# Optimization experiments

Hardware: AMD Instinct MI355X
Metric: run time of the kernel (lower is better)

The kernel has to match this reference:

```python
import jax, jax.numpy as jnp
import numpy as np

B, GRID, IN_CO, OUT_CO = 32, 4096, 64, 64
T_EMB, N_MODES = 256, 512
M_HALF = N_MODES // 2 + 1  # 257 retained rFFT modes


def setup_inputs() -> dict:
    key = jax.random.key(0)
    ks = jax.random.split(key, 6)
    w_std = jnp.sqrt(1.0 / (2.0 * IN_CO))
    return {
        "x": jax.random.normal(ks[0], (B, GRID, IN_CO), jnp.float32),
        "t_emb": jax.random.normal(ks[1], (B, T_EMB), jnp.float32),
        "weights_real": jax.random.normal(ks[2], (M_HALF, IN_CO, OUT_CO), jnp.float32) * w_std,
        "weights_imag": jax.random.normal(ks[3], (M_HALF, IN_CO, OUT_CO), jnp.float32) * w_std,
        "dense_real": jax.random.normal(ks[4], (T_EMB, M_HALF), jnp.float32) * jnp.sqrt(1.0 / T_EMB),
        "dense_imag": jax.random.normal(ks[5], (T_EMB, M_HALF), jnp.float32) * jnp.sqrt(1.0 / T_EMB),
    }


def reference(x, t_emb, weights_real, weights_imag, dense_real, dense_imag):
    b, in_grid_sz, _ = x.shape
    m = weights_real.shape[0]  # n_modes//2 + 1
    weights = weights_real + 1j * weights_imag  # (m, in_co, out_co)
    # rFFT over the grid axis
    x_ft = jnp.fft.rfft(x, axis=-2, norm="forward")  # (b, grid//2+1, in_co) complex
    # time modulation per mode: Dense(real) + i*Dense(imag)
    t_tr = (t_emb @ dense_real) + 1j * (t_emb @ dense_imag)  # (b, m)
    # original einsum with eye == elementwise per-mode scale then per-mode matmul
    x_out = jnp.einsum("bmi,mio->bmo", x_ft[:, :m, :], weights) * t_tr[:, :, None]
    out_ft = jnp.zeros((b, in_grid_sz // 2 + 1, weights.shape[-1]), jnp.complex64)
    out_ft = out_ft.at[:, :m, :].set(x_out)
    return jnp.fft.irfft(out_ft, axis=-2, n=in_grid_sz, norm="forward")
```

## Files before the change

### kernel.cpp

```cpp
#include <hip/hip_runtime.h>
#include <hip/hip_bf16.h>

typedef short short8 __attribute__((ext_vector_type(8)));
typedef float f32x4 __attribute__((ext_vector_type(4)));
typedef const void __attribute__((address_space(1))) as1_void;
typedef void __attribute__((address_space(3))) as3_void;

__device__ __forceinline__ float sin_rev(float r) {
  float o; asm("v_sin_f32 %0, %1" : "=v"(o) : "v"(r)); return o;
}
__device__ __forceinline__ float cos_rev(float r) {
  float o; asm("v_cos_f32 %0, %1" : "=v"(o) : "v"(r)); return o;
}

#define INV4096 0.000244140625f
#define INV16   0.0625f

__global__ __launch_bounds__(256) void prep_kernel(__hip_bfloat16* __restrict__ F2,
                                                   __hip_bfloat16* __restrict__ Gm,
                                                   const float* __restrict__ t_emb,
                                                   const float* __restrict__ dr,
                                                   const float* __restrict__ di,
                                                   float* __restrict__ Sr,
                                                   float* __restrict__ Si,
                                                   const float* __restrict__ x,
                                                   __hip_bfloat16* __restrict__ X2T,
                                                   float* __restrict__ Xr256p) {
  const int bid = blockIdx.x;
  const int tid = threadIdx.x;
  __shared__ float te[256];
  __shared__ float tile[64][65];
  __shared__ float red[4][64];

  if (bid < 512) {
    const int row = bid;
    const int m   = (row < 256) ? row : (row - 255);
    const bool is_cos = (row < 256);
#pragma unroll
    for (int it = 0; it < 2; ++it) {
      int n0 = it * 2048 + tid * 8;
      union { short8 v; unsigned short u[8]; } pk;
#pragma unroll
      for (int j = 0; j < 8; ++j) {
        int ph = (m * (n0 + j)) & 4095;
        float v = is_cos ?  cos_rev((float)ph * INV4096)
                         : -sin_rev((float)ph * INV4096);
        __hip_bfloat16 h = __float2bfloat16(v);
        pk.u[j] = *(unsigned short*)&h;
      }
      *(short8*)&F2[(size_t)row * 4096 + n0] = pk.v;
    }
  } else if (bid < 1024) {
    const int nb = (bid - 512) * 8;
#pragma unroll
    for (int it = 0; it < 2; ++it) {
      int e  = it * 2048 + tid * 8;
      int n  = nb + (e >> 9);
      int k0 = e & 511;
      union { short8 v; unsigned short u[8]; } pk;
#pragma unroll
      for (int j = 0; j < 8; ++j) {
        int kk = k0 + j;
        int m  = (kk < 256) ? kk : (kk - 255);
        int ph = (m * n) & 4095;
        float v = (kk < 256) ?  cos_rev((float)ph * INV4096)
                             : -sin_rev((float)ph * INV4096);
        __hip_bfloat16 h = __float2bfloat16(v);
        pk.u[j] = *(unsigned short*)&h;
      }
      *(short8*)&Gm[(size_t)n * 512 + k0] = pk.v;
    }
  } else if (bid < 1056) {
    int b = bid - 1024;
    te[tid] = t_emb[b * 256 + tid];
    __syncthreads();
    for (int m = tid; m < 257; m += 256) {
      float ar = 0.f, ai = 0.f;
      for (int t = 0; t < 256; ++t) {
        float e = te[t];
        ar += e * dr[t * 257 + m];
        ai += e * di[t * 257 + m];
      }
      float c = (m == 0 ? 1.0f : 2.0f) * (1.0f / 4096.0f);
      Sr[b * 257 + m] = ar * c;
      Si[b * 257 + m] = ai * c;
    }
  } else {
    int idx = bid - 1056;
    int nt = idx & 63;
    int b  = idx >> 6;
    int n0 = nt * 64;
#pragma unroll
    for (int it = 0; it < 4; ++it) {
      int c = it * 256 + tid;
      int r = c >> 4, i4 = (c & 15) * 4;
      float4 v = *(const float4*)&x[((size_t)b * 4096 + n0 + r) * 64 + i4];
      tile[r][i4 + 0] = v.x; tile[r][i4 + 1] = v.y;
      tile[r][i4 + 2] = v.z; tile[r][i4 + 3] = v.w;
    }
    __syncthreads();
#pragma unroll
    for (int it = 0; it < 2; ++it) {
      int c  = it * 256 + tid;
      int i  = c >> 3;
      int ch = c & 7;
      union { short8 v; unsigned short u[8]; } pk;
#pragma unroll
      for (int j = 0; j < 8; ++j) {
        __hip_bfloat16 h = __float2bfloat16(tile[ch * 8 + j][i]);
        pk.u[j] = *(unsigned short*)&h;
      }
      *(short8*)&X2T[((size_t)b * 64 + i) * 4096 + n0 + ch * 8] = pk.v;
    }
    {
      int i = tid & 63, g = tid >> 6;
      float acc = 0.f;
#pragma unroll
      for (int j = 0; j < 16; ++j)
        acc += cos_rev((float)j * INV16) * tile[g * 16 + j][i];
      red[g][i] = acc;
    }
    __syncthreads();
    if (tid < 64) {
      Xr256p[((size_t)b * 64 + nt) * 64 + tid] =
          red[0][tid] + red[1][tid] + red[2][tid] + red[3][tid];
    }
  }
}

__device__ __forceinline__ void gemm_core(const __hip_bfloat16* __restrict__ A, int lda, int m0,
                                          const __hip_bfloat16* __restrict__ B, int ldb, int n0,
                                          int k0, int ksteps,
                                          __hip_bfloat16* As, __hip_bfloat16* Bs,
                                          f32x4 acc[4][4]) {
  const int tid  = threadIdx.x;
  const int lane = tid & 63;
  const int wv   = tid >> 6;
  const int wr   = (wv >> 1) * 64;
  const int wc   = (wv & 1) * 64;
  const int fr   = lane & 15;
  const int fq   = lane >> 4;

  for (int ks = 0; ks < ksteps; ++ks) {
    int kt = k0 + ks * 64;
#pragma unroll
    for (int j = 0; j < 4; ++j) {
      int c   = j * 256 + tid;
      int row = c >> 3;
      int chg = (c & 7) ^ (row & 7);
      const __hip_bfloat16* ga = A + (size_t)(m0 + row) * lda + kt + chg * 8;
      const __hip_bfloat16* gb = B + (size_t)(n0 + row) * ldb + kt + chg * 8;
      __hip_bfloat16* la = As + (size_t)(j * 256 + (tid & 192)) * 8;
      __hip_bfloat16* lb = Bs + (size_t)(j * 256 + (tid & 192)) * 8;
      __builtin_amdgcn_global_load_lds((as1_void*)ga, (as3_void*)la, 16, 0, 0);
      __builtin_amdgcn_global_load_lds((as1_void*)gb, (as3_void*)lb, 16, 0, 0);
    }
    __syncthreads();
#pragma unroll
    for (int kk = 0; kk < 2; ++kk) {
      short8 av[4], bv[4];
#pragma unroll
      for (int m = 0; m < 4; ++m) {
        int row  = wr + m * 16 + fr;
        int slot = (fq + kk * 4) ^ (row & 7);
        av[m] = *(const short8*)(As + row * 64 + slot * 8);
      }
#pragma unroll
      for (int n = 0; n < 4; ++n) {
        int row  = wc + n * 16 + fr;
        int slot = (fq + kk * 4) ^ (row & 7);
        bv[n] = *(const short8*)(Bs + row * 64 + slot * 8);
      }
#pragma unroll
      for (int m = 0; m < 4; ++m)
#pragma unroll
        for (int n = 0; n < 4; ++n)
          acc[m][n] = __builtin_amdgcn_mfma_f32_16x16x32_bf16(av[m], bv[n], acc[m][n], 0, 0, 0);
    }
    __syncthreads();
  }
}

__global__ __launch_bounds__(256) void gemm1_kernel(const __hip_bfloat16* __restrict__ F2,
                                                    const __hip_bfloat16* __restrict__ X2T,
                                                    __hip_bfloat16* __restrict__ C1, int kchunk) {
  __shared__ __hip_bfloat16 As[128 * 64];
  __shared__ __hip_bfloat16 Bs[128 * 64];
  int n0 = blockIdx.x * 128;
  int m0 = blockIdx.y * 128;
  int k0 = blockIdx.z * kchunk;
  f32x4 acc[4][4];
#pragma unroll
  for (int m = 0; m < 4; ++m)
#pragma unroll
    for (int n = 0; n < 4; ++n)
#pragma unroll
      for (int r = 0; r < 4; ++r) acc[m][n][r] = 0.f;

  gemm_core(F2, 4096, m0, X2T, 4096, n0, k0, kchunk >> 6, As, Bs, acc);

  const int lane = threadIdx.x & 63;
  const int wv   = threadIdx.x >> 6;
  const int wr   = (wv >> 1) * 64, wc = (wv & 1) * 64;
  const int fr   = lane & 15, fq = lane >> 4;
  __hip_bfloat16* P = C1 + (size_t)blockIdx.z * (512 * 2048);
#pragma unroll
  for (int m = 0; m < 4; ++m)
#pragma unroll
    for (int n = 0; n < 4; ++n)
#pragma unroll
      for (int j = 0; j < 4; ++j) {
        int row = m0 + wr + m * 16 + fq * 4 + j;
        int col = n0 + wc + n * 16 + fr;
        P[(size_t)row * 2048 + col] = __float2bfloat16(acc[m][n][j]);
      }
}

__global__ __launch_bounds__(256) void mix_kernel(const __hip_bfloat16* __restrict__ C1,
                                                  const float* __restrict__ Xr256p,
                                                  const float* __restrict__ Wr,
                                                  const float* __restrict__ Wi,
                                                  const float* __restrict__ Sr,
                                                  const float* __restrict__ Si,
                                                  __hip_bfloat16* __restrict__ Y2T,
                                                  __hip_bfloat16* __restrict__ Yx,
                                                  int splitk) {
  const int k = blockIdx.x;
  const int q = blockIdx.y;
  const int tid = threadIdx.x;
  __shared__ float wlr[4096];
  __shared__ float wli[4096];
  __shared__ float xs[1024];

  const float* wrg = Wr + (size_t)k * 4096;
  const float* wig = Wi + (size_t)k * 4096;
  for (int c = tid; c < 1024; c += 256) {
    *(float4*)&wlr[c * 4] = *(const float4*)&wrg[c * 4];
    *(float4*)&wli[c * 4] = *(const float4*)&wig[c * 4];
  }
  const size_t PST = 512ull * 2048;
  for (int idx = tid; idx < 1024; idx += 256) {
    int part = idx >> 9;
    int c    = idx & 511;
    float s = 0.f;
    if (part == 0) {
      if (k < 256) {
        const __hip_bfloat16* src = C1 + (size_t)k * 2048 + q * 512 + c;
        for (int z = 0; z < splitk; ++z) s += __bfloat162float(src[(size_t)z * PST]);
      } else {
        int bi = q * 512 + c;
        const float* sp = Xr256p + (size_t)(bi >> 6) * 4096 + (bi & 63);
#pragma unroll 8
        for (int nt = 0; nt < 64; ++nt) s += sp[nt * 64];
      }
    } else if (k > 0) {
      const __hip_bfloat16* src = C1 + (size_t)(255 + k) * 2048 + q * 512 + c;
      for (int z = 0; z < splitk; ++z) s += __bfloat162float(src[(size_t)z * PST]);
    }
    xs[idx] = s;
  }
  __syncthreads();

  const int o  = tid & 63;
  const int jj = tid >> 6;
  const int bl0 = jj * 2, bl1 = jj * 2 + 1;
  float pr0 = 0.f, pi0 = 0.f, pr1 = 0.f, pi1 = 0.f;
#pragma unroll 8
  for (int i = 0; i < 64; ++i) {
    float wrv = wlr[i * 64 + o];
    float wiv = wli[i * 64 + o];
    float xr0 = xs[bl0 * 64 + i], xi0 = xs[512 + bl0 * 64 + i];
    float xr1 = xs[bl1 * 64 + i], xi1 = xs[512 + bl1 * 64 + i];
    pr0 += xr0 * wrv - xi0 * wiv;
    pi0 += xr0 * wiv + xi0 * wrv;
    pr1 += xr1 * wrv - xi1 * wiv;
    pi1 += xr1 * wiv + xi1 * wrv;
  }
  int b0 = q * 8 + bl0, b1 = q * 8 + bl1;
  float sr0 = Sr[b0 * 257 + k], si0 = Si[b0 * 257 + k];
  float sr1 = Sr[b1 * 257 + k], si1 = Si[b1 * 257 + k];
  int bo0 = b0 * 64 + o, bo1 = b1 * 64 + o;
  __hip_bfloat16 yr0 = __float2bfloat16(pr0 * sr0 - pi0 * si0);
  __hip_bfloat16 yi0 = __float2bfloat16(pr0 * si0 + pi0 * sr0);
  __hip_bfloat16 yr1 = __float2bfloat16(pr1 * sr1 - pi1 * si1);
  __hip_bfloat16 yi1 = __float2bfloat16(pr1 * si1 + pi1 * sr1);
  if (k < 256) {
    Y2T[(size_t)bo0 * 512 + k] = yr0;
    Y2T[(size_t)bo1 * 512 + k] = yr1;
  } else {
    Yx[bo0] = yr0;
    Yx[bo1] = yr1;
  }
  if (k >= 1) {
    Y2T[(size_t)bo0 * 512 + 255 + k] = yi0;
    Y2T[(size_t)bo1 * 512 + 255 + k] = yi1;
  }
}

__global__ __launch_bounds__(256) void gemm2_kernel(const __hip_bfloat16* __restrict__ Gm,
                                                    const __hip_bfloat16* __restrict__ Y2T,
                                                    const __hip_bfloat16* __restrict__ Yx,
                                                    float* __restrict__ out) {
  __shared__ __hip_bfloat16 As[128 * 64];
  __shared__ __hip_bfloat16 Bs[128 * 64];
  int n0 = blockIdx.x * 128;
  int m0 = blockIdx.y * 128;
  f32x4 acc[4][4];
#pragma unroll
  for (int m = 0; m < 4; ++m)
#pragma unroll
    for (int n = 0; n < 4; ++n)
#pragma unroll
      for (int r = 0; r < 4; ++r) acc[m][n][r] = 0.f;

  gemm_core(Gm, 512, m0, Y2T, 512, n0, 0, 8, As, Bs, acc);

  const int lane = threadIdx.x & 63;
  const int wv   = threadIdx.x >> 6;
  const int wr   = (wv >> 1) * 64, wc = (wv & 1) * 64;
  const int fr   = lane & 15, fq = lane >> 4;
  float yx[4];
#pragma unroll
  for (int n = 0; n < 4; ++n)
    yx[n] = __bfloat162float(Yx[n0 + wc + n * 16 + fr]);
#pragma unroll
  for (int m = 0; m < 4; ++m)
#pragma unroll
    for (int j = 0; j < 4; ++j) {
      int row = m0 + wr + m * 16 + fq * 4 + j;
      float g = cos_rev((float)(row & 15) * INV16);
#pragma unroll
      for (int n = 0; n < 4; ++n) {
        int col = n0 + wc + n * 16 + fr;
        int b = col >> 6, o = col & 63;
        out[((size_t)b * 4096 + row) * 64 + o] = acc[m][n][j] + g * yx[n];
      }
    }
}

extern "C" void kernel_launch(void* const* d_in, const int* in_sizes, int n_in,
                              void* d_out, int out_size, void* d_ws, size_t ws_size,
                              hipStream_t stream) {
  const float* x  = (const float*)d_in[0];
  const float* te = (const float*)d_in[1];
  const float* wr = (const float*)d_in[2];
  const float* wi = (const float*)d_in[3];
  const float* dr = (const float*)d_in[4];
  const float* di = (const float*)d_in[5];
  float* out = (float*)d_out;

  char* p = (char*)d_ws;
  auto alloc = [&](size_t bytes) -> char* {
    char* r = p;
    p += (bytes + 255) & ~(size_t)255;
    return r;
  };
  __hip_bfloat16* F2  = (__hip_bfloat16*)alloc(512ull * 4096 * 2);
  __hip_bfloat16* Gm  = (__hip_bfloat16*)alloc(4096ull * 512 * 2);
  __hip_bfloat16* X2T = (__hip_bfloat16*)alloc(2048ull * 4096 * 2);
  float* Xr256p = (float*)alloc(32ull * 64 * 64 * 4);
  float* Sr = (float*)alloc(32 * 257 * 4);
  float* Si = (float*)alloc(32 * 257 * 4);
  __hip_bfloat16* Y2T = (__hip_bfloat16*)alloc(2048ull * 512 * 2);
  __hip_bfloat16* Yx  = (__hip_bfloat16*)alloc(2048 * 2);
  size_t fixed = (size_t)(p - (char*)d_ws);

  int splitk = 1;
  if (ws_size >= fixed + 8ull * 512 * 2048 * 2)      splitk = 8;
  else if (ws_size >= fixed + 4ull * 512 * 2048 * 2) splitk = 4;
  else if (ws_size >= fixed + 2ull * 512 * 2048 * 2) splitk = 2;
  __hip_bfloat16* C1 = (__hip_bfloat16*)alloc((size_t)splitk * 512 * 2048 * 2);
  int kchunk = 4096 / splitk;

  prep_kernel<<<3104, 256, 0, stream>>>(F2, Gm, te, dr, di, Sr, Si, x, X2T, Xr256p);
  gemm1_kernel<<<dim3(16, 4, splitk), 256, 0, stream>>>(F2, X2T, C1, kchunk);
  mix_kernel<<<dim3(257, 4), 256, 0, stream>>>(C1, Xr256p, wr, wi, Sr, Si, Y2T, Yx, splitk);
  gemm2_kernel<<<dim3(16, 32), 256, 0, stream>>>(Gm, Y2T, Yx, out);
}
```

Baseline: 94.47 us.

## Double-buffer LDS tiles in shared GEMM core to overlap loads with MFMA

The shared GEMM core now keeps two LDS buffers per operand. It issues the global-to-LDS loads for the next k-tile before running the MFMA work on the current tile, and the two buffers swap each step. This is meant to hide global load latency behind compute and removes one of the two barriers per k-step. In exchange LDS use per block doubles to 64KB, which may cut occupancy. It relies on the single remaining barrier to cover completion of the async global_load_lds writes.

```diff
diff --git a/kernel.cpp b/kernel.cpp
--- a/kernel.cpp
+++ b/kernel.cpp
@@ -128,10 +128,55 @@
   }
 }
 
+__device__ __forceinline__ void stage_tile(const __hip_bfloat16* __restrict__ A, int lda, int m0,
+                                           const __hip_bfloat16* __restrict__ B, int ldb, int n0,
+                                           int kt, __hip_bfloat16* As, __hip_bfloat16* Bs,
+                                           int tid) {
+#pragma unroll
+  for (int j = 0; j < 4; ++j) {
+    int c   = j * 256 + tid;
+    int row = c >> 3;
+    int chg = (c & 7) ^ (row & 7);
+    const __hip_bfloat16* ga = A + (size_t)(m0 + row) * lda + kt + chg * 8;
+    const __hip_bfloat16* gb = B + (size_t)(n0 + row) * ldb + kt + chg * 8;
+    __hip_bfloat16* la = As + (size_t)(j * 256 + (tid & 192)) * 8;
+    __hip_bfloat16* lb = Bs + (size_t)(j * 256 + (tid & 192)) * 8;
+    __builtin_amdgcn_global_load_lds((as1_void*)ga, (as3_void*)la, 16, 0, 0);
+    __builtin_amdgcn_global_load_lds((as1_void*)gb, (as3_void*)lb, 16, 0, 0);
+  }
+}
+
+__device__ __forceinline__ void compute_step(const __hip_bfloat16* As, const __hip_bfloat16* Bs,
+                                             int wr, int wc, int fr, int fq,
+                                             f32x4 acc[4][4]) {
+#pragma unroll
+  for (int kk = 0; kk < 2; ++kk) {
+    short8 av[4], bv[4];
+#pragma unroll
+    for (int m = 0; m < 4; ++m) {
+      int row  = wr + m * 16 + fr;
+      int slot = (fq + kk * 4) ^ (row & 7);
+      av[m] = *(const short8*)(As + row * 64 + slot * 8);
+    }
+#pragma unroll
+    for (int n = 0; n < 4; ++n) {
+      int row  = wc + n * 16 + fr;
+      int slot = (fq + kk * 4) ^ (row & 7);
+      bv[n] = *(const short8*)(Bs + row * 64 + slot * 8);
+    }
+#pragma unroll
+    for (int m = 0; m < 4; ++m)
+#pragma unroll
+      for (int n = 0; n < 4; ++n)
+        acc[m][n] = __builtin_amdgcn_mfma_f32_16x16x32_bf16(av[m], bv[n], acc[m][n], 0, 0, 0);
+  }
+}
+
 __device__ __forceinline__ void gemm_core(const __hip_bfloat16* __restrict__ A, int lda, int m0,
                                           const __hip_bfloat16* __restrict__ B, int ldb, int n0,
                                           int k0, int ksteps,
-                                          __hip_bfloat16* As, __hip_bfloat16* Bs,
+                                          __hip_bfloat16* As0, __hip_bfloat16* Bs0,
+                                          __hip_bfloat16* As1, __hip_bfloat16* Bs1,
                                           f32x4 acc[4][4]) {
   const int tid  = threadIdx.x;
   const int lane = tid & 63;
@@ -141,51 +186,28 @@
   const int fr   = lane & 15;
   const int fq   = lane >> 4;
 
+  stage_tile(A, lda, m0, B, ldb, n0, k0, As0, Bs0, tid);
+  __syncthreads();
+
+  __hip_bfloat16 *Ac = As0, *Bc = Bs0, *An = As1, *Bn = Bs1;
   for (int ks = 0; ks < ksteps; ++ks) {
-    int kt = k0 + ks * 64;
-#pragma unroll
-    for (int j = 0; j < 4; ++j) {
-      int c   = j * 256 + tid;
-      int row = c >> 3;
-      int chg = (c & 7) ^ (row & 7);
-      const __hip_bfloat16* ga = A + (size_t)(m0 + row) * lda + kt + chg * 8;
-      const __hip_bfloat16* gb = B + (size_t)(n0 + row) * ldb + kt + chg * 8;
-      __hip_bfloat16* la = As + (size_t)(j * 256 + (tid & 192)) * 8;
-      __hip_bfloat16* lb = Bs + (size_t)(j * 256 + (tid & 192)) * 8;
-      __builtin_amdgcn_global_load_lds((as1_void*)ga, (as3_void*)la, 16, 0, 0);
-      __builtin_amdgcn_global_load_lds((as1_void*)gb, (as3_void*)lb, 16, 0, 0);
-    }
+    if (ks + 1 < ksteps)
+      stage_tile(A, lda, m0, B, ldb, n0, k0 + (ks + 1) * 64, An, Bn, tid);
+    compute_step(Ac, Bc, wr, wc, fr, fq, acc);
     __syncthreads();
-#pragma unroll
-    for (int kk = 0; kk < 2; ++kk) {
-      short8 av[4], bv[4];
-#pragma unroll
-      for (int m = 0; m < 4; ++m) {
-        int row  = wr + m * 16 + fr;
-        int slot = (fq + kk * 4) ^ (row & 7);
-        av[m] = *(const short8*)(As + row * 64 + slot * 8);
-      }
-#pragma unroll
-      for (int n = 0; n < 4; ++n) {
-        int row  = wc + n * 16 + fr;
-        int slot = (fq + kk * 4) ^ (row & 7);
-        bv[n] = *(const short8*)(Bs + row * 64 + slot * 8);
-      }
-#pragma unroll
-      for (int m = 0; m < 4; ++m)
-#pragma unroll
-        for (int n = 0; n < 4; ++n)
-          acc[m][n] = __builtin_amdgcn_mfma_f32_16x16x32_bf16(av[m], bv[n], acc[m][n], 0, 0, 0);
-    }
-    __syncthreads();
+    __hip_bfloat16* t;
+    t = Ac; Ac = An; An = t;
+    t = Bc; Bc = Bn; Bn = t;
   }
 }
 
 __global__ __launch_bounds__(256) void gemm1_kernel(const __hip_bfloat16* __restrict__ F2,
                                                     const __hip_bfloat16* __restrict__ X2T,
                                                     __hip_bfloat16* __restrict__ C1, int kchunk) {
-  __shared__ __hip_bfloat16 As[128 * 64];
-  __shared__ __hip_bfloat16 Bs[128 * 64];
+  __shared__ __hip_bfloat16 As0[128 * 64];
+  __shared__ __hip_bfloat16 Bs0[128 * 64];
+  __shared__ __hip_bfloat16 As1[128 * 64];
+  __shared__ __hip_bfloat16 Bs1[128 * 64];
   int n0 = blockIdx.x * 128;
   int m0 = blockIdx.y * 128;
   int k0 = blockIdx.z * kchunk;
@@ -197,7 +219,7 @@
 #pragma unroll
       for (int r = 0; r < 4; ++r) acc[m][n][r] = 0.f;
 
-  gemm_core(F2, 4096, m0, X2T, 4096, n0, k0, kchunk >> 6, As, Bs, acc);
+  gemm_core(F2, 4096, m0, X2T, 4096, n0, k0, kchunk >> 6, As0, Bs0, As1, Bs1, acc);
 
   const int lane = threadIdx.x & 63;
   const int wv   = threadIdx.x >> 6;
@@ -301,8 +323,10 @@
                                                     const __hip_bfloat16* __restrict__ Y2T,
                                                     const __hip_bfloat16* __restrict__ Yx,
                                                     float* __restrict__ out) {
-  __shared__ __hip_bfloat16 As[128 * 64];
-  __shared__ __hip_bfloat16 Bs[128 * 64];
+  __shared__ __hip_bfloat16 As0[128 * 64];
+  __shared__ __hip_bfloat16 Bs0[128 * 64];
+  __shared__ __hip_bfloat16 As1[128 * 64];
+  __shared__ __hip_bfloat16 Bs1[128 * 64];
   int n0 = blockIdx.x * 128;
   int m0 = blockIdx.y * 128;
   f32x4 acc[4][4];
@@ -313,7 +337,7 @@
 #pragma unroll
       for (int r = 0; r < 4; ++r) acc[m][n][r] = 0.f;
 
-  gemm_core(Gm, 512, m0, Y2T, 512, n0, 0, 8, As, Bs, acc);
+  gemm_core(Gm, 512, m0, Y2T, 512, n0, 0, 8, As0, Bs0, As1, Bs1, acc);
 
   const int lane = threadIdx.x & 63;
   const int wv   = threadIdx.x >> 6;
```

Measured after the change: 90.87 us. 3.8% less time.
